# Performance work log

Measured on AMD Instinct MI355X. Metric: run time of the kernel, lower is better.

Reference implementation:

```python
import jax, jax.numpy as jnp
import numpy as np

B = 262144
I = 128  # input_size
H = 128  # hidden_size


def setup_inputs() -> dict:
    key = jax.random.key(0)
    ks = jax.random.split(key, 12)
    std = 1.0 / np.sqrt(H)
    u = lambda k, shape: jax.random.uniform(k, shape, jnp.float32, -std, std)
    return {
        "inputs": jax.random.normal(ks[0], (B, I), jnp.float32),
        "h_prev": jax.random.normal(ks[1], (B, H), jnp.float32),
        "c_prev": jax.random.normal(ks[2], (B, H), jnp.float32),
        "W_ii": u(ks[3], (H, I)), "W_hi": u(ks[4], (H, H)),
        "W_if": u(ks[5], (H, I)), "W_hf": u(ks[6], (H, H)),
        "W_io": u(ks[7], (H, I)), "W_ho": u(ks[8], (H, H)),
        "W_ig": u(ks[9], (H, I)), "W_hg": u(ks[10], (H, H)),
    }


def reference(inputs, h_prev, c_prev, W_ii, W_hi, W_if, W_hf, W_io, W_ho, W_ig, W_hg):
    # Same math as 8 separate GEMMs, expressed as 2 fused GEMMs over concatenated gates.
    W_x = jnp.concatenate([W_ii, W_if, W_io, W_ig], axis=0)  # [4H, I]
    W_h = jnp.concatenate([W_hi, W_hf, W_ho, W_hg], axis=0)  # [4H, H]
    gates = inputs @ W_x.T + h_prev @ W_h.T  # [B, 4H]
    gi, gf, go, gg = jnp.split(gates, 4, axis=-1)
    i_t = jax.nn.sigmoid(gi)
    f_t = jax.nn.sigmoid(gf)
    o_t = jax.nn.sigmoid(go)
    g_t = jnp.tanh(gg)
    c_t = f_t * c_prev + i_t * g_t
    h_t = o_t * jnp.tanh(c_t)
    return jnp.stack([h_t, c_t], axis=0)  # [2, B, H]
```

## Files before the change

kernel.cpp:

```cpp
#include <hip/hip_runtime.h>

#define BATCH 262144
#define NBLK 512
#define NITER 32
#define ROWS 32
#define ASTRIDE 264
#define BH 33554432

typedef __attribute__((ext_vector_type(8))) short bf16x8;
typedef __attribute__((ext_vector_type(4))) float f32x4;
typedef __attribute__((ext_vector_type(8))) unsigned short u16x8;

__device__ __forceinline__ unsigned short f2bf(float f) {
  unsigned int u = __float_as_uint(f);
  u += 0x7fffu + ((u >> 16) & 1u);
  return (unsigned short)(u >> 16);
}

__device__ __forceinline__ float fexp(float x) { return __builtin_amdgcn_exp2f(x * 1.44269504f); }
__device__ __forceinline__ float sigm(float x) { return __builtin_amdgcn_rcpf(1.f + fexp(-x)); }
__device__ __forceinline__ float ftanh(float x) { return 1.f - 2.f * __builtin_amdgcn_rcpf(1.f + fexp(2.f * x)); }

__global__ __launch_bounds__(256, 2) void lstm_fused(
    const float* __restrict__ X, const float* __restrict__ H0, const float* __restrict__ C0,
    const float* __restrict__ Wii, const float* __restrict__ Whi,
    const float* __restrict__ Wif, const float* __restrict__ Whf,
    const float* __restrict__ Wio, const float* __restrict__ Who,
    const float* __restrict__ Wig, const float* __restrict__ Whg,
    float* __restrict__ Out) {
  __shared__ __align__(16) unsigned short Abuf[2][ROWS * ASTRIDE];

  const int tid = threadIdx.x;
  const int wave = tid >> 6;
  const int lane = tid & 63;
  const int lrow = lane & 15;
  const int lkq = lane >> 4;

  const int bid = blockIdx.x;
  const int xcd = bid & 7;
  const int ch = (bid >> 3) & 1;
  const int p = bid >> 4;
  const int tbase = p + 32 * xcd;
  const int colbase = ch * 64 + wave * 16;
  const int hcol = colbase + lrow;

  const float* Wxp[4] = {Wii, Wif, Wio, Wig};
  const float* Whp[4] = {Whi, Whf, Who, Whg};

  bf16x8 wf[4][8];
#pragma unroll
  for (int g = 0; g < 4; ++g) {
#pragma unroll
    for (int kk = 0; kk < 8; ++kk) {
      const int k = kk * 32 + lkq * 8;
      const float* src = (kk < 4) ? (Wxp[g] + hcol * 128 + k)
                                  : (Whp[g] + hcol * 128 + (k - 128));
      float4 lo = *(const float4*)src;
      float4 hi = *(const float4*)(src + 4);
      bf16x8 w;
      w[0] = (short)f2bf(lo.x); w[1] = (short)f2bf(lo.y);
      w[2] = (short)f2bf(lo.z); w[3] = (short)f2bf(lo.w);
      w[4] = (short)f2bf(hi.x); w[5] = (short)f2bf(hi.y);
      w[6] = (short)f2bf(hi.z); w[7] = (short)f2bf(hi.w);
      wf[g][kk] = w;
    }
  }

  const int r0 = tid >> 4;
  const int ci = tid & 15;
  const int coff = ci * 16;
  float4 s0, s1, s2, s3, s4, s5, s6, s7;
  f32x4 cv0, cv1;

#define ISSUE_LOADS(ROW0) do {                                            \
    const float* pA_ = (ci < 8)                                           \
        ? (X + (size_t)((ROW0) + r0) * 128 + ci * 16)                     \
        : (H0 + (size_t)((ROW0) + r0) * 128 + (ci - 8) * 16);             \
    s0 = ((const float4*)pA_)[0];  s1 = ((const float4*)pA_)[1];          \
    s2 = ((const float4*)pA_)[2];  s3 = ((const float4*)pA_)[3];          \
    const float* pB_ = pA_ + 16 * 128;                                    \
    s4 = ((const float4*)pB_)[0];  s5 = ((const float4*)pB_)[1];          \
    s6 = ((const float4*)pB_)[2];  s7 = ((const float4*)pB_)[3];          \
  } while (0)

#define CVT8(DST, A, B) do {                                              \
    u16x8 t_;                                                             \
    t_[0] = f2bf((A).x); t_[1] = f2bf((A).y);                             \
    t_[2] = f2bf((A).z); t_[3] = f2bf((A).w);                             \
    t_[4] = f2bf((B).x); t_[5] = f2bf((B).y);                             \
    t_[6] = f2bf((B).z); t_[7] = f2bf((B).w);                             \
    *(u16x8*)(DST) = t_;                                                  \
  } while (0)

#define MT(MT_, CV, AB, ROW0) do {                                        \
    f32x4 a0 = {0.f, 0.f, 0.f, 0.f}, a1 = a0, a2 = a0, a3 = a0;           \
    _Pragma("unroll")                                                     \
    for (int kk = 0; kk < 8; ++kk) {                                      \
      bf16x8 b_ = *(const bf16x8*)&(AB)[((MT_)*16 + lrow) * ASTRIDE + kk * 32 + lkq * 8]; \
      a0 = __builtin_amdgcn_mfma_f32_16x16x32_bf16(wf[0][kk], b_, a0, 0, 0, 0); \
      a1 = __builtin_amdgcn_mfma_f32_16x16x32_bf16(wf[1][kk], b_, a1, 0, 0, 0); \
      a2 = __builtin_amdgcn_mfma_f32_16x16x32_bf16(wf[2][kk], b_, a2, 0, 0, 0); \
      a3 = __builtin_amdgcn_mfma_f32_16x16x32_bf16(wf[3][kk], b_, a3, 0, 0, 0); \
    }                                                                     \
    f32x4 hv_, cf_;                                                       \
    _Pragma("unroll")                                                     \
    for (int j = 0; j < 4; ++j) {                                         \
      const float itv = sigm(a0[j]);                                      \
      const float ftv = sigm(a1[j]);                                      \
      const float otv = sigm(a2[j]);                                      \
      const float gtv = ftanh(a3[j]);                                     \
      const float ctv = ftv * (CV)[j] + itv * gtv;                        \
      cf_[j] = ctv;                                                       \
      hv_[j] = otv * ftanh(ctv);                                          \
    }                                                                     \
    const size_t ob_ = (size_t)((ROW0) + (MT_)*16 + lrow) * 128 + colbase + lkq * 4; \
    __builtin_nontemporal_store(hv_, (f32x4*)(Out + ob_));                \
    __builtin_nontemporal_store(cf_, (f32x4*)(Out + BH + ob_));           \
  } while (0)

#define BODY(IT, AB) do {                                                 \
    const int row0_ = (tbase + (IT) * 256) * ROWS;                        \
                          \
    CVT8(&(AB)[r0 * ASTRIDE + coff], s0, s1);                             \
    CVT8(&(AB)[r0 * ASTRIDE + coff + 8], s2, s3);                         \
    CVT8(&(AB)[(r0 + 16) * ASTRIDE + coff], s4, s5);                      \
    CVT8(&(AB)[(r0 + 16) * ASTRIDE + coff + 8], s6, s7);                  \
    __syncthreads();         \
       \
       \
                                            \
    cv0 = __builtin_nontemporal_load(                                     \
        (const f32x4*)(C0 + (size_t)(row0_ + lrow) * 128 + colbase + lkq * 4));      \
    cv1 = __builtin_nontemporal_load(                                     \
        (const f32x4*)(C0 + (size_t)(row0_ + 16 + lrow) * 128 + colbase + lkq * 4)); \
    if ((IT) + 1 < NITER) ISSUE_LOADS(row0_ + 256 * ROWS);                \
    MT(0, cv0, AB, row0_);                                                \
    MT(1, cv1, AB, row0_);                                                \
  } while (0)

  ISSUE_LOADS(tbase * ROWS);

  for (int it = 0; it < NITER; it += 2) {
    BODY(it, &Abuf[0][0]);
    BODY(it + 1, &Abuf[1][0]);
  }

#undef ISSUE_LOADS
#undef CVT8
#undef MT
#undef BODY
}

extern "C" void kernel_launch(void* const* d_in, const int* in_sizes, int n_in,
                              void* d_out, int out_size, void* d_ws, size_t ws_size,
                              hipStream_t stream) {
  (void)in_sizes; (void)n_in; (void)out_size; (void)d_ws; (void)ws_size;
  lstm_fused<<<NBLK, 256, 0, stream>>>(
      (const float*)d_in[0], (const float*)d_in[1], (const float*)d_in[2],
      (const float*)d_in[3], (const float*)d_in[4], (const float*)d_in[5],
      (const float*)d_in[6], (const float*)d_in[7], (const float*)d_in[8],
      (const float*)d_in[9], (const float*)d_in[10],
      (float*)d_out);
}
```

Measured before the change: 166.5 us.

## Stream X/H tiles directly into LDS via global_load_lds with swizzled fp32 layout

Replaces the register-staged load, bf16 convert and LDS store with direct global-to-LDS DMA loads (global_load_lds) of fp32 tiles, using an XOR swizzle to avoid bank conflicts. The bf16 conversion moves into the MFMA loop, so each of the eight waves converts the shared B operand again. Blocks grow to 512 threads covering all 128 hidden columns, with 256 blocks each handling a contiguous row range. The XCD-aware block mapping and nontemporal stores are dropped. This trades register pressure and staging latency for doubled LDS footprint and redundant per-wave conversion work.

Measured after the change: 168.5 us. No clear change (+1.2%).

```diff
diff --git a/kernel.cpp b/kernel.cpp
--- a/kernel.cpp
+++ b/kernel.cpp
@@ -1,15 +1,12 @@
 #include <hip/hip_runtime.h>
 
-#define BATCH 262144
-#define NBLK 512
+#define NBLK 256
 #define NITER 32
 #define ROWS 32
-#define ASTRIDE 264
 #define BH 33554432
 
 typedef __attribute__((ext_vector_type(8))) short bf16x8;
 typedef __attribute__((ext_vector_type(4))) float f32x4;
-typedef __attribute__((ext_vector_type(8))) unsigned short u16x8;
 
 __device__ __forceinline__ unsigned short f2bf(float f) {
   unsigned int u = __float_as_uint(f);
@@ -21,31 +18,45 @@
 __device__ __forceinline__ float sigm(float x) { return __builtin_amdgcn_rcpf(1.f + fexp(-x)); }
 __device__ __forceinline__ float ftanh(float x) { return 1.f - 2.f * __builtin_amdgcn_rcpf(1.f + fexp(2.f * x)); }
 
-__global__ __launch_bounds__(256, 2) void lstm_fused(
+#define GLOAD_LDS(G, L) __builtin_amdgcn_global_load_lds(                 \
+    (const __attribute__((address_space(1))) unsigned int*)(G),           \
+    (__attribute__((address_space(3))) unsigned int*)(L), 16, 0, 0)
+
+__global__ __launch_bounds__(512, 2) void lstm_fused(
     const float* __restrict__ X, const float* __restrict__ H0, const float* __restrict__ C0,
     const float* __restrict__ Wii, const float* __restrict__ Whi,
     const float* __restrict__ Wif, const float* __restrict__ Whf,
     const float* __restrict__ Wio, const float* __restrict__ Who,
     const float* __restrict__ Wig, const float* __restrict__ Whg,
     float* __restrict__ Out) {
-  __shared__ __align__(16) unsigned short Abuf[2][ROWS * ASTRIDE];
+  __shared__ __align__(16) float Buf[2][ROWS * 256];
 
   const int tid = threadIdx.x;
-  const int wave = tid >> 6;
+  const int wid = tid >> 6;
   const int lane = tid & 63;
   const int lrow = lane & 15;
   const int lkq = lane >> 4;
+  const int s = lrow & 7;
+  const int colw = wid * 16;
 
-  const int bid = blockIdx.x;
-  const int xcd = bid & 7;
-  const int ch = (bid >> 3) & 1;
-  const int p = bid >> 4;
-  const int tbase = p + 32 * xcd;
-  const int colbase = ch * 64 + wave * 16;
-  const int hcol = colbase + lrow;
+  const int row_base = blockIdx.x * (NITER * ROWS);
 
   const float* Wxp[4] = {Wii, Wif, Wio, Wig};
   const float* Whp[4] = {Whi, Whf, Who, Whg};
+
+#define GLDS_TILE(ROW0, BUFP) do {                                        \
+    _Pragma("unroll")                                                     \
+    for (int j_ = 0; j_ < 4; ++j_) {                                      \
+      const int q_ = wid * 4 + j_;                   \
+      const int cs_ = lane ^ (q_ & 7);         \
+      const float* g_ = (cs_ < 32)                                        \
+          ? (X + (size_t)((ROW0) + q_) * 128 + cs_ * 4)                   \
+          : (H0 + (size_t)((ROW0) + q_) * 128 + (cs_ - 32) * 4);          \
+      GLOAD_LDS(g_, (BUFP) + q_ * 256);            \
+    }                                                                     \
+  } while (0)
+
+  GLDS_TILE(row_base, &Buf[0][0]);
 
   bf16x8 wf[4][8];
 #pragma unroll
@@ -53,8 +64,8 @@
 #pragma unroll
     for (int kk = 0; kk < 8; ++kk) {
       const int k = kk * 32 + lkq * 8;
-      const float* src = (kk < 4) ? (Wxp[g] + hcol * 128 + k)
-                                  : (Whp[g] + hcol * 128 + (k - 128));
+      const float* src = (kk < 4) ? (Wxp[g] + (size_t)(colw + lrow) * 128 + k)
+                                  : (Whp[g] + (size_t)(colw + lrow) * 128 + (k - 128));
       float4 lo = *(const float4*)src;
       float4 hi = *(const float4*)(src + 4);
       bf16x8 w;
@@ -65,38 +76,22 @@
       wf[g][kk] = w;
     }
   }
+  __syncthreads();
 
-  const int r0 = tid >> 4;
-  const int ci = tid & 15;
-  const int coff = ci * 16;
-  float4 s0, s1, s2, s3, s4, s5, s6, s7;
-  f32x4 cv0, cv1;
-
-#define ISSUE_LOADS(ROW0) do {                                            \
-    const float* pA_ = (ci < 8)                                           \
-        ? (X + (size_t)((ROW0) + r0) * 128 + ci * 16)                     \
-        : (H0 + (size_t)((ROW0) + r0) * 128 + (ci - 8) * 16);             \
-    s0 = ((const float4*)pA_)[0];  s1 = ((const float4*)pA_)[1];          \
-    s2 = ((const float4*)pA_)[2];  s3 = ((const float4*)pA_)[3];          \
-    const float* pB_ = pA_ + 16 * 128;                                    \
-    s4 = ((const float4*)pB_)[0];  s5 = ((const float4*)pB_)[1];          \
-    s6 = ((const float4*)pB_)[2];  s7 = ((const float4*)pB_)[3];          \
-  } while (0)
-
-#define CVT8(DST, A, B) do {                                              \
-    u16x8 t_;                                                             \
-    t_[0] = f2bf((A).x); t_[1] = f2bf((A).y);                             \
-    t_[2] = f2bf((A).z); t_[3] = f2bf((A).w);                             \
-    t_[4] = f2bf((B).x); t_[5] = f2bf((B).y);                             \
-    t_[6] = f2bf((B).z); t_[7] = f2bf((B).w);                             \
-    *(u16x8*)(DST) = t_;                                                  \
-  } while (0)
-
-#define MT(MT_, CV, AB, ROW0) do {                                        \
+#define MT(MT_, CV, CUR, ROW0) do {                                       \
     f32x4 a0 = {0.f, 0.f, 0.f, 0.f}, a1 = a0, a2 = a0, a3 = a0;           \
+    const float* bp_ = (CUR) + ((MT_)*16 + lrow) * 256;                   \
+    const int o0_ = ((lkq * 2) ^ s) * 4;                                  \
+    const int o1_ = o0_ ^ 4;                                              \
     _Pragma("unroll")                                                     \
     for (int kk = 0; kk < 8; ++kk) {                                      \
-      bf16x8 b_ = *(const bf16x8*)&(AB)[((MT_)*16 + lrow) * ASTRIDE + kk * 32 + lkq * 8]; \
+      f32x4 u_ = *(const f32x4*)(bp_ + kk * 32 + o0_);                    \
+      f32x4 v_ = *(const f32x4*)(bp_ + kk * 32 + o1_);                    \
+      bf16x8 b_;                                                          \
+      b_[0] = (short)f2bf(u_[0]); b_[1] = (short)f2bf(u_[1]);             \
+      b_[2] = (short)f2bf(u_[2]); b_[3] = (short)f2bf(u_[3]);             \
+      b_[4] = (short)f2bf(v_[0]); b_[5] = (short)f2bf(v_[1]);             \
+      b_[6] = (short)f2bf(v_[2]); b_[7] = (short)f2bf(v_[3]);             \
       a0 = __builtin_amdgcn_mfma_f32_16x16x32_bf16(wf[0][kk], b_, a0, 0, 0, 0); \
       a1 = __builtin_amdgcn_mfma_f32_16x16x32_bf16(wf[1][kk], b_, a1, 0, 0, 0); \
       a2 = __builtin_amdgcn_mfma_f32_16x16x32_bf16(wf[2][kk], b_, a2, 0, 0, 0); \
@@ -104,58 +99,47 @@
     }                                                                     \
     f32x4 hv_, cf_;                                                       \
     _Pragma("unroll")                                                     \
-    for (int j = 0; j < 4; ++j) {                                         \
-      const float itv = sigm(a0[j]);                                      \
-      const float ftv = sigm(a1[j]);                                      \
-      const float otv = sigm(a2[j]);                                      \
-      const float gtv = ftanh(a3[j]);                                     \
-      const float ctv = ftv * (CV)[j] + itv * gtv;                        \
-      cf_[j] = ctv;                                                       \
-      hv_[j] = otv * ftanh(ctv);                                          \
+    for (int j_ = 0; j_ < 4; ++j_) {                                      \
+      const float itv = sigm(a0[j_]);                                     \
+      const float ftv = sigm(a1[j_]);                                     \
+      const float otv = sigm(a2[j_]);                                     \
+      const float gtv = ftanh(a3[j_]);                                    \
+      const float ctv = ftv * (CV)[j_] + itv * gtv;                       \
+      cf_[j_] = ctv;                                                      \
+      hv_[j_] = otv * ftanh(ctv);                                         \
     }                                                                     \
-    const size_t ob_ = (size_t)((ROW0) + (MT_)*16 + lrow) * 128 + colbase + lkq * 4; \
-    __builtin_nontemporal_store(hv_, (f32x4*)(Out + ob_));                \
-    __builtin_nontemporal_store(cf_, (f32x4*)(Out + BH + ob_));           \
+    const size_t ob_ = (size_t)((ROW0) + (MT_)*16 + lrow) * 128 + colw + lkq * 4; \
+    *(f32x4*)(Out + ob_) = hv_;                                           \
+    *(f32x4*)(Out + BH + ob_) = cf_;                                      \
   } while (0)
 
-#define BODY(IT, AB) do {                                                 \
-    const int row0_ = (tbase + (IT) * 256) * ROWS;                        \
-                          \
-    CVT8(&(AB)[r0 * ASTRIDE + coff], s0, s1);                             \
-    CVT8(&(AB)[r0 * ASTRIDE + coff + 8], s2, s3);                         \
-    CVT8(&(AB)[(r0 + 16) * ASTRIDE + coff], s4, s5);                      \
-    CVT8(&(AB)[(r0 + 16) * ASTRIDE + coff + 8], s6, s7);                  \
-    __syncthreads();         \
-       \
-       \
-                                            \
-    cv0 = __builtin_nontemporal_load(                                     \
-        (const f32x4*)(C0 + (size_t)(row0_ + lrow) * 128 + colbase + lkq * 4));      \
-    cv1 = __builtin_nontemporal_load(                                     \
-        (const f32x4*)(C0 + (size_t)(row0_ + 16 + lrow) * 128 + colbase + lkq * 4)); \
-    if ((IT) + 1 < NITER) ISSUE_LOADS(row0_ + 256 * ROWS);                \
-    MT(0, cv0, AB, row0_);                                                \
-    MT(1, cv1, AB, row0_);                                                \
+#define ITER(T, CUR, NXT) do {                                            \
+    const int row0_ = row_base + (T) * ROWS;                              \
+     \
+                             \
+    f32x4 cva_ = *(const f32x4*)(C0 + (size_t)(row0_ + lrow) * 128 + colw + lkq * 4);      \
+    f32x4 cvb_ = *(const f32x4*)(C0 + (size_t)(row0_ + 16 + lrow) * 128 + colw + lkq * 4); \
+    if ((T) + 1 < NITER) GLDS_TILE(row0_ + ROWS, NXT);                    \
+    MT(0, cva_, CUR, row0_);                                              \
+    MT(1, cvb_, CUR, row0_);                                              \
+    __syncthreads();           \
   } while (0)
 
-  ISSUE_LOADS(tbase * ROWS);
-
-  for (int it = 0; it < NITER; it += 2) {
-    BODY(it, &Abuf[0][0]);
-    BODY(it + 1, &Abuf[1][0]);
+  for (int t = 0; t < NITER; t += 2) {
+    ITER(t, &Buf[0][0], &Buf[1][0]);
+    ITER(t + 1, &Buf[1][0], &Buf[0][0]);
   }
 
-#undef ISSUE_LOADS
-#undef CVT8
+#undef GLDS_TILE
 #undef MT
-#undef BODY
+#undef ITER
 }
 
 extern "C" void kernel_launch(void* const* d_in, const int* in_sizes, int n_in,
                               void* d_out, int out_size, void* d_ws, size_t ws_size,
                               hipStream_t stream) {
   (void)in_sizes; (void)n_in; (void)out_size; (void)d_ws; (void)ws_size;
-  lstm_fused<<<NBLK, 256, 0, stream>>>(
+  lstm_fused<<<NBLK, 512, 0, stream>>>(
       (const float*)d_in[0], (const float*)d_in[1], (const float*)d_in[2],
       (const float*)d_in[3], (const float*)d_in[4], (const float*)d_in[5],
       (const float*)d_in[6], (const float*)d_in[7], (const float*)d_in[8],
```
